# Performance work log

Hardware: AMD Instinct MI355X
Metric: run time of the kernel (lower is better)

The kernel has to match this reference:

```python
import jax, jax.numpy as jnp
import numpy as np
import math

N_HEAD = 4
NORM_GROUPS = 16
EPS = 1e-5


def setup_inputs() -> dict:
    key = jax.random.key(0)
    ks = jax.random.split(key, 4)
    B, C, H, W = 2, 256, 64, 64
    return {
        "input": jax.random.normal(ks[0], (B, C, H, W), dtype=jnp.float32),
        "gn_weight": jnp.ones((C,), dtype=jnp.float32),
        "gn_bias": jnp.zeros((C,), dtype=jnp.float32),
        # 1x1 convs are plain channel matmuls: weight [out_ch, in_ch]
        "qkv_weight": jax.random.normal(ks[1], (3 * C, C), dtype=jnp.float32) / math.sqrt(C),
        "out_weight": jax.random.normal(ks[2], (C, C), dtype=jnp.float32) / math.sqrt(C),
        "out_bias": jnp.zeros((C,), dtype=jnp.float32),
    }


def _group_norm(x, weight, bias):
    B, C, H, W = x.shape
    g = x.reshape(B, NORM_GROUPS, C // NORM_GROUPS, H, W)
    mu = g.mean(axis=(2, 3, 4), keepdims=True)
    var = g.var(axis=(2, 3, 4), keepdims=True)
    g = (g - mu) * jax.lax.rsqrt(var + EPS)
    return g.reshape(B, C, H, W) * weight[:, None, None] + bias[:, None, None]


def reference(input, gn_weight, gn_bias, qkv_weight, out_weight, out_bias):
    B, C, H, W = input.shape
    head_dim = C // N_HEAD
    x = _group_norm(input, gn_weight, gn_bias)
    # 1x1 conv (no bias) -> [B, 3C, H, W] -> [B, n_head, 3*head_dim, H, W]
    qkv = jnp.einsum('bchw,oc->bohw', x, qkv_weight)
    qkv = qkv.reshape(B, N_HEAD, 3 * head_dim, H, W)
    q, k, v = jnp.split(qkv, 3, axis=2)
    # full spatial attention; note: scale is sqrt(channel), as in the source
    attn = jnp.einsum('bnchw,bncyx->bnhwyx', q, k) / math.sqrt(C)
    attn = jax.nn.softmax(attn.reshape(B, N_HEAD, H, W, H * W), axis=-1)
    attn = attn.reshape(B, N_HEAD, H, W, H, W)
    out = jnp.einsum('bnhwyx,bncyx->bnchw', attn, v).reshape(B, C, H, W)
    out = jnp.einsum('bchw,oc->bohw', out, out_weight) + out_bias[:, None, None]
    return out + input
```

## Files before the change

### kernel.cpp

```cpp
#include <hip/hip_runtime.h>

typedef __bf16        bf16x8 __attribute__((ext_vector_type(8)));
typedef float         f32x4  __attribute__((ext_vector_type(4)));
typedef unsigned short u16x4 __attribute__((ext_vector_type(4)));
typedef unsigned short u16x8 __attribute__((ext_vector_type(8)));
typedef unsigned int  u32x4  __attribute__((ext_vector_type(4)));

#define MFMA16(a,b,c) __builtin_amdgcn_mfma_f32_16x16x32_bf16((a),(b),(c),0,0,0)

static __device__ __forceinline__ unsigned short f2bf(float f) {
  unsigned int u = __builtin_bit_cast(unsigned int, f);
  u += 0x7fffu + ((u >> 16) & 1u);
  return (unsigned short)(u >> 16);
}
static __device__ __forceinline__ unsigned int pk2(float a, float b) {
  unsigned int ua = __builtin_bit_cast(unsigned int, a) + 0x8000u;
  unsigned int ub = __builtin_bit_cast(unsigned int, b) + 0x8000u;
  return __builtin_amdgcn_perm(ub, ua, 0x07060302u);
}
static __device__ __forceinline__ unsigned int pk2rne(float a, float b) {
  return (unsigned int)f2bf(a) | ((unsigned int)f2bf(b) << 16);
}
static __device__ __forceinline__ bf16x8 as_bf(u32x4 v) {
  return __builtin_bit_cast(bf16x8, v);
}
static __device__ __forceinline__ float bf2f(unsigned short u) {
  return __builtin_bit_cast(float, ((unsigned int)u) << 16);
}
static __device__ __forceinline__ void dma16(const unsigned short* g, unsigned short* l) {
  __builtin_amdgcn_global_load_lds((const __attribute__((address_space(1))) unsigned int*)g,
                                   (__attribute__((address_space(3))) unsigned int*)l, 16, 0, 0);
}

#define SDIM 4096
#define CDIM 256
#define NHEAD 4
#define HDIM 64
#define NBATCH 2
#define KSPLIT 4

__global__ __launch_bounds__(256) void k_prep(const float* __restrict__ x,
                                              const float* __restrict__ wq,
                                              const float* __restrict__ wo,
                                              unsigned short* __restrict__ wqb,
                                              unsigned short* __restrict__ wob,
                                              float2* __restrict__ Sp) {
  int j = blockIdx.x, i = threadIdx.x;
  if (j < 256) {
    const float* p = x + (size_t)(j >> 3) * 65536 + (size_t)(j & 7) * 8192;
    float s = 0.f, sq = 0.f;
#pragma unroll
    for (int r = 0; r < 8; ++r) {
      float4 v = *(const float4*)(p + (r * 256 + i) * 4);
      s  += v.x + v.y + v.z + v.w;
      sq += v.x * v.x + v.y * v.y + v.z * v.z + v.w * v.w;
    }
    __shared__ float rs[256], rq[256];
    rs[i] = s; rq[i] = sq;
    __syncthreads();
    for (int off = 128; off > 0; off >>= 1) {
      if (i < off) { rs[i] += rs[i + off]; rq[i] += rq[i + off]; }
      __syncthreads();
    }
    if (i == 0) Sp[j] = make_float2(rs[0], rq[0]);
  } else {
    int t = (j - 256) * 256 + i;
    int e = t * 16;
#pragma unroll
    for (int c = 0; c < 4; ++c) {
      int idx = e + c * 4;
      const float* src = (idx < 768 * 256) ? (wq + idx) : (wo + idx - 768 * 256);
      unsigned short* dst = (idx < 768 * 256) ? (wqb + idx) : (wob + idx - 768 * 256);
      float4 v = *(const float4*)src;
      u16x4 r; r[0] = f2bf(v.x); r[1] = f2bf(v.y); r[2] = f2bf(v.z); r[3] = f2bf(v.w);
      *(u16x4*)dst = r;
    }
  }
}

__global__ __launch_bounds__(256) void k_gn_apply(const float* __restrict__ x,
                                                  const float2* __restrict__ Sp,
                                                  const float* __restrict__ gnw,
                                                  const float* __restrict__ gnb,
                                                  unsigned short* __restrict__ xn) {
  __shared__ __attribute__((aligned(16))) unsigned short sT[64 * 268];
  __shared__ float2 sStat[16];
  int b = blockIdx.y, s0 = blockIdx.x * 64;
  int i = threadIdx.x, lane = i & 63, w = i >> 6;
  if (i < 16) {
    float s = 0.f, sq = 0.f;
#pragma unroll
    for (int u = 0; u < 8; ++u) {
      float2 v = Sp[(b * 16 + i) * 8 + u];
      s += v.x; sq += v.y;
    }
    float mean = s * (1.f / 65536.f);
    float var  = sq * (1.f / 65536.f) - mean * mean;
    sStat[i] = make_float2(mean, rsqrtf(var + 1e-5f));
  }
  __syncthreads();
#pragma unroll 4
  for (int r = 0; r < 64; ++r) {
    int c = r * 4 + w;
    float v = x[((size_t)(b * CDIM + c)) * SDIM + s0 + lane];
    float2 st = sStat[c >> 4];
    float nv = (v - st.x) * st.y * gnw[c] + gnb[c];
    sT[lane * 268 + c] = f2bf(nv);
  }
  __syncthreads();
#pragma unroll
  for (int r = 0; r < 16; ++r) {
    int sl = r * 4 + w;
    u16x4 v = *(const u16x4*)&sT[sl * 268 + lane * 4];
    *(u16x4*)&xn[((size_t)(b * SDIM + s0 + sl)) * CDIM + lane * 4] = v;
  }
}

template <int M, int MODE>
__global__ __launch_bounds__(256) void k_gemm(const unsigned short* __restrict__ W,
                                              const unsigned short* __restrict__ X,
                                              unsigned short* __restrict__ Qf,
                                              unsigned short* __restrict__ Kf,
                                              unsigned short* __restrict__ Vf,
                                              float* __restrict__ outf,
                                              const float* __restrict__ bias,
                                              const float* __restrict__ resid) {
  __shared__ __attribute__((aligned(16))) unsigned short sX[64 * 40];
  __shared__ __attribute__((aligned(16))) unsigned short sB[64 * 68];
  int b = blockIdx.z, s0 = blockIdx.y * 64, o0 = blockIdx.x * 64;
  int i = threadIdx.x, lane = i & 63, w = i >> 6;
  int quad = lane >> 4, m = lane & 15;
  const unsigned short* Xb = X + ((size_t)b * SDIM + s0) * CDIM;
  int ss = i >> 2, cq = i & 3;

  f32x4 acc[4] = {};
#pragma unroll
  for (int k0 = 0; k0 < 256; k0 += 32) {
    u32x4 xv = *(const u32x4*)(Xb + ss * CDIM + k0 + cq * 8);
    *(u32x4*)&sX[ss * 40 + cq * 8] = xv;
    __syncthreads();
    bf16x8 a = as_bf(*(const u32x4*)(W + (o0 + w * 16 + m) * 256 + k0 + quad * 8));
#pragma unroll
    for (int st = 0; st < 4; ++st) {
      bf16x8 bx = as_bf(*(const u32x4*)&sX[(st * 16 + m) * 40 + quad * 8]);
      acc[st] = MFMA16(a, bx, acc[st]);
    }
    __syncthreads();
  }
  if (MODE == 1) {
#pragma unroll
    for (int st = 0; st < 4; ++st)
#pragma unroll
      for (int r = 0; r < 4; ++r) {
        int o = o0 + w * 16 + quad * 4 + r;
        int s = s0 + st * 16 + m;
        size_t idx = ((size_t)b * M + o) * SDIM + s;
        outf[idx] = acc[st][r] + bias[o] + resid[idx];
      }
  } else {
    int sec = (o0 >> 6) % 3;
    int h   = o0 / 192;
    int bh  = b * NHEAD + h;
    float qs = (sec == 0) ? 0.09016844f : 1.0f;
#pragma unroll
    for (int st = 0; st < 4; ++st) {
      uint2 pk = make_uint2(pk2rne(acc[st][0] * qs, acc[st][1] * qs),
                            pk2rne(acc[st][2] * qs, acc[st][3] * qs));
      *(uint2*)&sB[(st * 16 + m) * 68 + w * 16 + quad * 4] = pk;
    }
    __syncthreads();
    int lp = i & 63, qp = lp >> 4, mp = lp & 15, t = i >> 6;
    if (sec < 2) {
      unsigned short* base = (sec == 0) ? Qf : Kf;
#pragma unroll
      for (int ks = 0; ks < 2; ++ks) {
        const unsigned short* src = &sB[(t * 16 + mp) * 68 + ks * 32 + qp * 8];
        u16x4 lo = *(const u16x4*)src;
        u16x4 hi = *(const u16x4*)(src + 4);
        unsigned short* dst = base + ((((size_t)bh * 256 + (s0 >> 4) + t) * 2 + ks) * 64 + lp) * 8;
        *(u16x4*)dst = lo;
        *(u16x4*)(dst + 4) = hi;
      }
    } else {
      int kt32l = t >> 1, dts = (t & 1) * 2;
#pragma unroll
      for (int dd = 0; dd < 2; ++dd) {
        int dt = dts + dd;
        u16x8 v;
#pragma unroll
        for (int jj = 0; jj < 8; ++jj)
          v[jj] = sB[(kt32l * 32 + qp * 8 + jj) * 68 + dt * 16 + mp];
        unsigned short* dst = Vf + ((((size_t)bh * 128 + (s0 >> 5) + kt32l) * 4 + dt) * 64 + lp) * 8;
        *(u16x8*)dst = v;
      }
    }
  }
}

__global__ __launch_bounds__(256, 4) void k_attn(const unsigned short* __restrict__ Qf,
                                                 const unsigned short* __restrict__ Kf,
                                                 const unsigned short* __restrict__ Vf,
                                                 unsigned short* __restrict__ Opb,
                                                 float* __restrict__ Lp) {
  __shared__ __attribute__((aligned(16))) unsigned short sK[2][2048];
  __shared__ __attribute__((aligned(16))) unsigned short sV[2][2048];
  __shared__ __attribute__((aligned(16))) unsigned short sP[4][32 * 40];
  int bh = blockIdx.y, kk = blockIdx.z;
  int i = threadIdx.x, lane = i & 63, w = i >> 6;
  int quad = lane >> 4, m = lane & 15;
  constexpr int ITERS = SDIM / KSPLIT / 32;

  bf16x8 bq[2][2];
#pragma unroll
  for (int qt = 0; qt < 2; ++qt)
#pragma unroll
    for (int ks = 0; ks < 2; ++ks)
      bq[qt][ks] = as_bf(*(const u32x4*)(Qf +
        ((((size_t)bh * 256 + (blockIdx.x * 8 + w * 2 + qt)) * 2 + ks) * 64 + lane) * 8));

  f32x4 oacc[2][4] = {};
  float li[2] = {0.f, 0.f};

  auto dma = [&](int it, int buf) {
    int kb16 = kk * (ITERS * 2) + it * 2 + (w >> 1);
    dma16(Kf + ((((size_t)bh * 256 + kb16) * 2 + (w & 1)) * 64 + lane) * 8,
          &sK[buf][w * 512]);
    int kb32 = kk * ITERS + it;
    dma16(Vf + ((((size_t)bh * 128 + kb32) * 4 + w) * 64 + lane) * 8,
          &sV[buf][w * 512]);
  };
  dma(0, 0);

  for (int it = 0; it < ITERS; ++it) {
    int buf = it & 1;
    __syncthreads();
    if (it < ITERS - 1) dma(it + 1, buf ^ 1);

    {
      bf16x8 ak[2][2];
#pragma unroll
      for (int ky = 0; ky < 2; ++ky)
#pragma unroll
        for (int ks = 0; ks < 2; ++ks)
          ak[ky][ks] = *(const bf16x8*)&sK[buf][((ky * 2 + ks) * 64 + lane) * 8];
#pragma unroll
      for (int qt = 0; qt < 2; ++qt) {
        f32x4 sc0 = {-18.f, -18.f, -18.f, -18.f};
        f32x4 sc1 = sc0;
        sc0 = MFMA16(ak[0][0], bq[qt][0], sc0);
        sc0 = MFMA16(ak[0][1], bq[qt][1], sc0);
        sc1 = MFMA16(ak[1][0], bq[qt][0], sc1);
        sc1 = MFMA16(ak[1][1], bq[qt][1], sc1);
        float p[8];
#pragma unroll
        for (int r = 0; r < 4; ++r) {
          p[r]     = __builtin_amdgcn_exp2f(sc0[r]);
          p[4 + r] = __builtin_amdgcn_exp2f(sc1[r]);
        }
        li[qt] += ((p[0] + p[1]) + (p[2] + p[3])) + ((p[4] + p[5]) + (p[6] + p[7]));
        int row = (qt * 16 + m) * 40;
        *(uint2*)&sP[w][row + quad * 4]      = make_uint2(pk2(p[0], p[1]), pk2(p[2], p[3]));
        *(uint2*)&sP[w][row + 16 + quad * 4] = make_uint2(pk2(p[4], p[5]), pk2(p[6], p[7]));
      }
    }
    {
      bf16x8 av[4];
#pragma unroll
      for (int dt = 0; dt < 4; ++dt)
        av[dt] = *(const bf16x8*)&sV[buf][(dt * 64 + lane) * 8];
#pragma unroll
      for (int qt = 0; qt < 2; ++qt) {
        bf16x8 bp = *(const bf16x8*)&sP[w][(qt * 16 + m) * 40 + quad * 8];
#pragma unroll
        for (int dt = 0; dt < 4; ++dt)
          oacc[qt][dt] = MFMA16(av[dt], bp, oacc[qt][dt]);
      }
    }
  }

  size_t qg = (size_t)(kk * 8 + bh) * SDIM + blockIdx.x * 128 + w * 32;
#pragma unroll
  for (int qt = 0; qt < 2; ++qt) {
    li[qt] += __shfl_xor(li[qt], 16);
    li[qt] += __shfl_xor(li[qt], 32);
  }
  if (quad == 0) {
#pragma unroll
    for (int qt = 0; qt < 2; ++qt) Lp[qg + qt * 16 + m] = li[qt];
  }
#pragma unroll
  for (int qt = 0; qt < 2; ++qt)
#pragma unroll
    for (int dt = 0; dt < 4; ++dt) {
      uint2 pk = make_uint2(pk2rne(oacc[qt][dt][0], oacc[qt][dt][1]),
                            pk2rne(oacc[qt][dt][2], oacc[qt][dt][3]));
      *(uint2*)&Opb[(qg + qt * 16 + m) * 64 + dt * 16 + quad * 4] = pk;
    }
}

__global__ __launch_bounds__(256) void k_combine(const unsigned short* __restrict__ Opb,
                                                 const float* __restrict__ Lp,
                                                 unsigned short* __restrict__ ao) {
  int gid = blockIdx.x * 256 + threadIdx.x;
  int bh = gid >> 14, rem = gid & 16383, q = rem >> 2, dq = rem & 3;
  float li = 0.f, o[16];
#pragma unroll
  for (int e = 0; e < 16; ++e) o[e] = 0.f;
#pragma unroll
  for (int ks = 0; ks < KSPLIT; ++ks) {
    size_t base = (size_t)(ks * 8 + bh) * SDIM + q;
    li += Lp[base];
    const unsigned short* p = Opb + base * 64 + dq * 16;
    u16x8 a = *(const u16x8*)p, b2 = *(const u16x8*)(p + 8);
#pragma unroll
    for (int e = 0; e < 8; ++e) { o[e] += bf2f(a[e]); o[8 + e] += bf2f(b2[e]); }
  }
  float inv = 1.f / li;
  unsigned int dw[8];
#pragma unroll
  for (int e = 0; e < 8; ++e) dw[e] = pk2rne(o[2 * e] * inv, o[2 * e + 1] * inv);
  unsigned short* dst = ao + ((size_t)((bh >> 2) * SDIM + q)) * CDIM + (bh & 3) * HDIM + dq * 16;
  *(u32x4*)dst       = u32x4{dw[0], dw[1], dw[2], dw[3]};
  *(u32x4*)(dst + 8) = u32x4{dw[4], dw[5], dw[6], dw[7]};
}

extern "C" void kernel_launch(void* const* d_in, const int* in_sizes, int n_in,
                              void* d_out, int out_size, void* d_ws, size_t ws_size,
                              hipStream_t stream) {
  const float* input = (const float*)d_in[0];
  const float* gnw   = (const float*)d_in[1];
  const float* gnb   = (const float*)d_in[2];
  const float* wq    = (const float*)d_in[3];
  const float* wo    = (const float*)d_in[4];
  const float* ob    = (const float*)d_in[5];
  float* out = (float*)d_out;

  char* ws = (char*)d_ws;
  unsigned short* xn  = (unsigned short*)(ws);
  unsigned short* Qf  = (unsigned short*)(ws + (4ull  << 20));
  unsigned short* Kf  = (unsigned short*)(ws + (8ull  << 20));
  unsigned short* Vf  = (unsigned short*)(ws + (12ull << 20));
  unsigned short* ao  = (unsigned short*)(ws + (16ull << 20));
  unsigned short* wqb = (unsigned short*)(ws + (20ull << 20));
  unsigned short* wob = (unsigned short*)(ws + (20ull << 20) + (1u << 19));
  float2* Sp          = (float2*)(ws + (20ull << 20) + (3u << 18));
  float* Lp           = (float*)(ws + (21ull << 20));
  unsigned short* Opb = (unsigned short*)(ws + (22ull << 20));

  k_prep<<<320, 256, 0, stream>>>(input, wq, wo, wqb, wob, Sp);
  k_gn_apply<<<dim3(64, NBATCH), 256, 0, stream>>>(input, Sp, gnw, gnb, xn);
  k_gemm<768, 0><<<dim3(12, 64, NBATCH), 256, 0, stream>>>(wqb, xn, Qf, Kf, Vf, nullptr, nullptr, nullptr);
  k_attn<<<dim3(32, NHEAD * NBATCH, KSPLIT), 256, 0, stream>>>(Qf, Kf, Vf, Opb, Lp);
  k_combine<<<512, 256, 0, stream>>>(Opb, Lp, ao);
  k_gemm<256, 1><<<dim3(4, 64, NBATCH), 256, 0, stream>>>(wob, ao, nullptr, nullptr, nullptr, out, ob, input);
}
```

Baseline: 147.0 us.

## Pre-swizzle operands into MFMA fragment layout and drop LDS staging

Weights, normalized activations and attention output are now written in a per-lane MFMA fragment layout, so the GEMMs load operands straight from global memory with no LDS staging or barriers. The attention kernel drops its double-buffered global-to-LDS K/V prefetch in favour of direct fragment loads. It computes the softmax row sum with an extra MFMA against a ones vector, which removes the exp-sum adds and cross-lane shuffles. It also uses the hardware packed bf16 conversion when available. In exchange, K/V global loads are no longer overlapped with compute, and the row sum is now taken from bf16-rounded probabilities.

```diff
diff --git a/kernel.cpp b/kernel.cpp
--- a/kernel.cpp
+++ b/kernel.cpp
@@ -13,23 +13,22 @@
   u += 0x7fffu + ((u >> 16) & 1u);
   return (unsigned short)(u >> 16);
 }
-static __device__ __forceinline__ unsigned int pk2(float a, float b) {
-  unsigned int ua = __builtin_bit_cast(unsigned int, a) + 0x8000u;
-  unsigned int ub = __builtin_bit_cast(unsigned int, b) + 0x8000u;
-  return __builtin_amdgcn_perm(ub, ua, 0x07060302u);
-}
 static __device__ __forceinline__ unsigned int pk2rne(float a, float b) {
   return (unsigned int)f2bf(a) | ((unsigned int)f2bf(b) << 16);
 }
+static __device__ __forceinline__ unsigned int pkrn(float a, float b) {
+#if __has_builtin(__builtin_amdgcn_cvt_pk_bf16_f32)
+  auto r = __builtin_amdgcn_cvt_pk_bf16_f32(a, b);
+  return __builtin_bit_cast(unsigned int, r);
+#else
+  return pk2rne(a, b);
+#endif
+}
 static __device__ __forceinline__ bf16x8 as_bf(u32x4 v) {
   return __builtin_bit_cast(bf16x8, v);
 }
 static __device__ __forceinline__ float bf2f(unsigned short u) {
   return __builtin_bit_cast(float, ((unsigned int)u) << 16);
-}
-static __device__ __forceinline__ void dma16(const unsigned short* g, unsigned short* l) {
-  __builtin_amdgcn_global_load_lds((const __attribute__((address_space(1))) unsigned int*)g,
-                                   (__attribute__((address_space(3))) unsigned int*)l, 16, 0, 0);
 }
 
 #define SDIM 4096
@@ -42,8 +41,8 @@
 __global__ __launch_bounds__(256) void k_prep(const float* __restrict__ x,
                                               const float* __restrict__ wq,
                                               const float* __restrict__ wo,
-                                              unsigned short* __restrict__ wqb,
-                                              unsigned short* __restrict__ wob,
+                                              unsigned short* __restrict__ wqf,
+                                              unsigned short* __restrict__ wof,
                                               float2* __restrict__ Sp) {
   int j = blockIdx.x, i = threadIdx.x;
   if (j < 256) {
@@ -65,15 +64,24 @@
     if (i == 0) Sp[j] = make_float2(rs[0], rq[0]);
   } else {
     int t = (j - 256) * 256 + i;
-    int e = t * 16;
-#pragma unroll
-    for (int c = 0; c < 4; ++c) {
-      int idx = e + c * 4;
-      const float* src = (idx < 768 * 256) ? (wq + idx) : (wo + idx - 768 * 256);
-      unsigned short* dst = (idx < 768 * 256) ? (wqb + idx) : (wob + idx - 768 * 256);
-      float4 v = *(const float4*)src;
-      u16x4 r; r[0] = f2bf(v.x); r[1] = f2bf(v.y); r[2] = f2bf(v.z); r[3] = f2bf(v.w);
-      *(u16x4*)dst = r;
+#pragma unroll
+    for (int u = 0; u < 2; ++u) {
+      int G = t * 2 + u;
+      const float* src; unsigned short* dst;
+      if (G < 24576) {
+        int tile = G >> 6, l = G & 63;
+        src = wq + (size_t)((tile >> 3) * 16 + (l & 15)) * 256 + (tile & 7) * 32 + (l >> 4) * 8;
+        dst = wqf + (size_t)G * 8;
+      } else {
+        int G2 = G - 24576, tile = G2 >> 6, l = G2 & 63;
+        src = wo + (size_t)((tile >> 3) * 16 + (l & 15)) * 256 + (tile & 7) * 32 + (l >> 4) * 8;
+        dst = wof + (size_t)G2 * 8;
+      }
+      float4 v0 = *(const float4*)src, v1 = *(const float4*)(src + 4);
+      u16x8 r;
+      r[0] = f2bf(v0.x); r[1] = f2bf(v0.y); r[2] = f2bf(v0.z); r[3] = f2bf(v0.w);
+      r[4] = f2bf(v1.x); r[5] = f2bf(v1.y); r[6] = f2bf(v1.z); r[7] = f2bf(v1.w);
+      *(u16x8*)dst = r;
     }
   }
 }
@@ -82,7 +90,7 @@
                                                   const float2* __restrict__ Sp,
                                                   const float* __restrict__ gnw,
                                                   const float* __restrict__ gnb,
-                                                  unsigned short* __restrict__ xn) {
+                                                  unsigned short* __restrict__ Xf) {
   __shared__ __attribute__((aligned(16))) unsigned short sT[64 * 268];
   __shared__ float2 sStat[16];
   int b = blockIdx.y, s0 = blockIdx.x * 64;
@@ -108,45 +116,45 @@
     sT[lane * 268 + c] = f2bf(nv);
   }
   __syncthreads();
-#pragma unroll
-  for (int r = 0; r < 16; ++r) {
-    int sl = r * 4 + w;
-    u16x4 v = *(const u16x4*)&sT[sl * 268 + lane * 4];
-    *(u16x4*)&xn[((size_t)(b * SDIM + s0 + sl)) * CDIM + lane * 4] = v;
+  int l = i & 63, fr = i >> 6;
+#pragma unroll
+  for (int g = 0; g < 8; ++g) {
+    int tile = fr * 8 + g, st = tile >> 3, kc = tile & 7;
+    const unsigned short* src = &sT[(st * 16 + (l & 15)) * 268 + kc * 32 + (l >> 4) * 8];
+    u16x4 lo = *(const u16x4*)src, hi = *(const u16x4*)(src + 4);
+    unsigned short* dst = Xf + (((size_t)(b * 256 + (s0 >> 4) + st) * 8 + kc) * 64 + l) * 8;
+    *(u16x4*)dst = lo;
+    *(u16x4*)(dst + 4) = hi;
   }
 }
 
 template <int M, int MODE>
-__global__ __launch_bounds__(256) void k_gemm(const unsigned short* __restrict__ W,
-                                              const unsigned short* __restrict__ X,
+__global__ __launch_bounds__(256) void k_gemm(const unsigned short* __restrict__ Wf,
+                                              const unsigned short* __restrict__ Xf,
                                               unsigned short* __restrict__ Qf,
                                               unsigned short* __restrict__ Kf,
                                               unsigned short* __restrict__ Vf,
                                               float* __restrict__ outf,
                                               const float* __restrict__ bias,
                                               const float* __restrict__ resid) {
-  __shared__ __attribute__((aligned(16))) unsigned short sX[64 * 40];
   __shared__ __attribute__((aligned(16))) unsigned short sB[64 * 68];
   int b = blockIdx.z, s0 = blockIdx.y * 64, o0 = blockIdx.x * 64;
   int i = threadIdx.x, lane = i & 63, w = i >> 6;
   int quad = lane >> 4, m = lane & 15;
-  const unsigned short* Xb = X + ((size_t)b * SDIM + s0) * CDIM;
-  int ss = i >> 2, cq = i & 3;
+  int ot = blockIdx.x * 4 + w;
+  int stg = s0 >> 4;
 
   f32x4 acc[4] = {};
 #pragma unroll
-  for (int k0 = 0; k0 < 256; k0 += 32) {
-    u32x4 xv = *(const u32x4*)(Xb + ss * CDIM + k0 + cq * 8);
-    *(u32x4*)&sX[ss * 40 + cq * 8] = xv;
-    __syncthreads();
-    bf16x8 a = as_bf(*(const u32x4*)(W + (o0 + w * 16 + m) * 256 + k0 + quad * 8));
+  for (int kc = 0; kc < 8; ++kc) {
+    bf16x8 aW = as_bf(*(const u32x4*)(Wf + (((size_t)ot * 8 + kc) * 64 + lane) * 8));
 #pragma unroll
     for (int st = 0; st < 4; ++st) {
-      bf16x8 bx = as_bf(*(const u32x4*)&sX[(st * 16 + m) * 40 + quad * 8]);
-      acc[st] = MFMA16(a, bx, acc[st]);
-    }
-    __syncthreads();
-  }
+      bf16x8 bX = as_bf(*(const u32x4*)(Xf + ((((size_t)b * 256 + stg + st) * 8 + kc) * 64 + lane) * 8));
+      acc[st] = MFMA16(aW, bX, acc[st]);
+    }
+  }
+
   if (MODE == 1) {
 #pragma unroll
     for (int st = 0; st < 4; ++st)
@@ -202,8 +210,6 @@
                                                  const unsigned short* __restrict__ Vf,
                                                  unsigned short* __restrict__ Opb,
                                                  float* __restrict__ Lp) {
-  __shared__ __attribute__((aligned(16))) unsigned short sK[2][2048];
-  __shared__ __attribute__((aligned(16))) unsigned short sV[2][2048];
   __shared__ __attribute__((aligned(16))) unsigned short sP[4][32 * 40];
   int bh = blockIdx.y, kk = blockIdx.z;
   int i = threadIdx.x, lane = i & 63, w = i >> 6;
@@ -218,75 +224,64 @@
       bq[qt][ks] = as_bf(*(const u32x4*)(Qf +
         ((((size_t)bh * 256 + (blockIdx.x * 8 + w * 2 + qt)) * 2 + ks) * 64 + lane) * 8));
 
+  bf16x8 aone;
+  {
+    u16x8 t;
+#pragma unroll
+    for (int jj = 0; jj < 8; ++jj) t[jj] = 0x3F80;
+    aone = __builtin_bit_cast(bf16x8, t);
+  }
+
   f32x4 oacc[2][4] = {};
-  float li[2] = {0.f, 0.f};
-
-  auto dma = [&](int it, int buf) {
-    int kb16 = kk * (ITERS * 2) + it * 2 + (w >> 1);
-    dma16(Kf + ((((size_t)bh * 256 + kb16) * 2 + (w & 1)) * 64 + lane) * 8,
-          &sK[buf][w * 512]);
+  f32x4 liacc[2] = {};
+
+  for (int it = 0; it < ITERS; ++it) {
+    bf16x8 ak[2][2], av[4];
+    int kb16 = kk * (ITERS * 2) + it * 2;
+#pragma unroll
+    for (int ky = 0; ky < 2; ++ky)
+#pragma unroll
+      for (int ks = 0; ks < 2; ++ks)
+        ak[ky][ks] = as_bf(*(const u32x4*)(Kf +
+          ((((size_t)bh * 256 + kb16 + ky) * 2 + ks) * 64 + lane) * 8));
     int kb32 = kk * ITERS + it;
-    dma16(Vf + ((((size_t)bh * 128 + kb32) * 4 + w) * 64 + lane) * 8,
-          &sV[buf][w * 512]);
-  };
-  dma(0, 0);
-
-  for (int it = 0; it < ITERS; ++it) {
-    int buf = it & 1;
-    __syncthreads();
-    if (it < ITERS - 1) dma(it + 1, buf ^ 1);
-
-    {
-      bf16x8 ak[2][2];
-#pragma unroll
-      for (int ky = 0; ky < 2; ++ky)
-#pragma unroll
-        for (int ks = 0; ks < 2; ++ks)
-          ak[ky][ks] = *(const bf16x8*)&sK[buf][((ky * 2 + ks) * 64 + lane) * 8];
-#pragma unroll
-      for (int qt = 0; qt < 2; ++qt) {
-        f32x4 sc0 = {-18.f, -18.f, -18.f, -18.f};
-        f32x4 sc1 = sc0;
-        sc0 = MFMA16(ak[0][0], bq[qt][0], sc0);
-        sc0 = MFMA16(ak[0][1], bq[qt][1], sc0);
-        sc1 = MFMA16(ak[1][0], bq[qt][0], sc1);
-        sc1 = MFMA16(ak[1][1], bq[qt][1], sc1);
-        float p[8];
-#pragma unroll
-        for (int r = 0; r < 4; ++r) {
-          p[r]     = __builtin_amdgcn_exp2f(sc0[r]);
-          p[4 + r] = __builtin_amdgcn_exp2f(sc1[r]);
-        }
-        li[qt] += ((p[0] + p[1]) + (p[2] + p[3])) + ((p[4] + p[5]) + (p[6] + p[7]));
-        int row = (qt * 16 + m) * 40;
-        *(uint2*)&sP[w][row + quad * 4]      = make_uint2(pk2(p[0], p[1]), pk2(p[2], p[3]));
-        *(uint2*)&sP[w][row + 16 + quad * 4] = make_uint2(pk2(p[4], p[5]), pk2(p[6], p[7]));
-      }
-    }
-    {
-      bf16x8 av[4];
+#pragma unroll
+    for (int dt = 0; dt < 4; ++dt)
+      av[dt] = as_bf(*(const u32x4*)(Vf +
+        ((((size_t)bh * 128 + kb32) * 4 + dt) * 64 + lane) * 8));
+
+#pragma unroll
+    for (int qt = 0; qt < 2; ++qt) {
+      f32x4 sc0 = {-18.f, -18.f, -18.f, -18.f};
+      f32x4 sc1 = sc0;
+      sc0 = MFMA16(ak[0][0], bq[qt][0], sc0);
+      sc0 = MFMA16(ak[0][1], bq[qt][1], sc0);
+      sc1 = MFMA16(ak[1][0], bq[qt][0], sc1);
+      sc1 = MFMA16(ak[1][1], bq[qt][1], sc1);
+      float p[8];
+#pragma unroll
+      for (int r = 0; r < 4; ++r) {
+        p[r]     = __builtin_amdgcn_exp2f(sc0[r]);
+        p[4 + r] = __builtin_amdgcn_exp2f(sc1[r]);
+      }
+      int row = (qt * 16 + m) * 40;
+      *(uint2*)&sP[w][row + quad * 4]      = make_uint2(pkrn(p[0], p[1]), pkrn(p[2], p[3]));
+      *(uint2*)&sP[w][row + 16 + quad * 4] = make_uint2(pkrn(p[4], p[5]), pkrn(p[6], p[7]));
+    }
+#pragma unroll
+    for (int qt = 0; qt < 2; ++qt) {
+      bf16x8 bp = *(const bf16x8*)&sP[w][(qt * 16 + m) * 40 + quad * 8];
 #pragma unroll
       for (int dt = 0; dt < 4; ++dt)
-        av[dt] = *(const bf16x8*)&sV[buf][(dt * 64 + lane) * 8];
-#pragma unroll
-      for (int qt = 0; qt < 2; ++qt) {
-        bf16x8 bp = *(const bf16x8*)&sP[w][(qt * 16 + m) * 40 + quad * 8];
-#pragma unroll
-        for (int dt = 0; dt < 4; ++dt)
-          oacc[qt][dt] = MFMA16(av[dt], bp, oacc[qt][dt]);
-      }
+        oacc[qt][dt] = MFMA16(av[dt], bp, oacc[qt][dt]);
+      liacc[qt] = MFMA16(aone, bp, liacc[qt]);
     }
   }
 
   size_t qg = (size_t)(kk * 8 + bh) * SDIM + blockIdx.x * 128 + w * 32;
-#pragma unroll
-  for (int qt = 0; qt < 2; ++qt) {
-    li[qt] += __shfl_xor(li[qt], 16);
-    li[qt] += __shfl_xor(li[qt], 32);
-  }
   if (quad == 0) {
 #pragma unroll
-    for (int qt = 0; qt < 2; ++qt) Lp[qg + qt * 16 + m] = li[qt];
+    for (int qt = 0; qt < 2; ++qt) Lp[qg + qt * 16 + m] = liacc[qt][0];
   }
 #pragma unroll
   for (int qt = 0; qt < 2; ++qt)
@@ -300,7 +295,7 @@
 
 __global__ __launch_bounds__(256) void k_combine(const unsigned short* __restrict__ Opb,
                                                  const float* __restrict__ Lp,
-                                                 unsigned short* __restrict__ ao) {
+                                                 unsigned short* __restrict__ aof) {
   int gid = blockIdx.x * 256 + threadIdx.x;
   int bh = gid >> 14, rem = gid & 16383, q = rem >> 2, dq = rem & 3;
   float li = 0.f, o[16];
@@ -319,9 +314,11 @@
   unsigned int dw[8];
 #pragma unroll
   for (int e = 0; e < 8; ++e) dw[e] = pk2rne(o[2 * e] * inv, o[2 * e + 1] * inv);
-  unsigned short* dst = ao + ((size_t)((bh >> 2) * SDIM + q)) * CDIM + (bh & 3) * HDIM + dq * 16;
-  *(u32x4*)dst       = u32x4{dw[0], dw[1], dw[2], dw[3]};
-  *(u32x4*)(dst + 8) = u32x4{dw[4], dw[5], dw[6], dw[7]};
+  int b = bh >> 2, c0 = (bh & 3) * 64 + dq * 16;
+  int st = q >> 4, mm = q & 15, kc = c0 >> 5, qd = (c0 >> 3) & 3;
+  unsigned short* base = aof + (((size_t)(b * 256 + st) * 8 + kc) * 64) * 8;
+  *(u32x4*)(base + (qd * 16 + mm) * 8)       = u32x4{dw[0], dw[1], dw[2], dw[3]};
+  *(u32x4*)(base + ((qd + 1) * 16 + mm) * 8) = u32x4{dw[4], dw[5], dw[6], dw[7]};
 }
 
 extern "C" void kernel_launch(void* const* d_in, const int* in_sizes, int n_in,
@@ -336,21 +333,21 @@
   float* out = (float*)d_out;
 
   char* ws = (char*)d_ws;
-  unsigned short* xn  = (unsigned short*)(ws);
+  unsigned short* Xf  = (unsigned short*)(ws);
   unsigned short* Qf  = (unsigned short*)(ws + (4ull  << 20));
   unsigned short* Kf  = (unsigned short*)(ws + (8ull  << 20));
   unsigned short* Vf  = (unsigned short*)(ws + (12ull << 20));
-  unsigned short* ao  = (unsigned short*)(ws + (16ull << 20));
-  unsigned short* wqb = (unsigned short*)(ws + (20ull << 20));
-  unsigned short* wob = (unsigned short*)(ws + (20ull << 20) + (1u << 19));
+  unsigned short* aof = (unsigned short*)(ws + (16ull << 20));
+  unsigned short* wqf = (unsigned short*)(ws + (20ull << 20));
+  unsigned short* wof = (unsigned short*)(ws + (20ull << 20) + (1u << 19));
   float2* Sp          = (float2*)(ws + (20ull << 20) + (3u << 18));
   float* Lp           = (float*)(ws + (21ull << 20));
   unsigned short* Opb = (unsigned short*)(ws + (22ull << 20));
 
-  k_prep<<<320, 256, 0, stream>>>(input, wq, wo, wqb, wob, Sp);
-  k_gn_apply<<<dim3(64, NBATCH), 256, 0, stream>>>(input, Sp, gnw, gnb, xn);
-  k_gemm<768, 0><<<dim3(12, 64, NBATCH), 256, 0, stream>>>(wqb, xn, Qf, Kf, Vf, nullptr, nullptr, nullptr);
+  k_prep<<<320, 256, 0, stream>>>(input, wq, wo, wqf, wof, Sp);
+  k_gn_apply<<<dim3(64, NBATCH), 256, 0, stream>>>(input, Sp, gnw, gnb, Xf);
+  k_gemm<768, 0><<<dim3(12, 64, NBATCH), 256, 0, stream>>>(wqf, Xf, Qf, Kf, Vf, nullptr, nullptr, nullptr);
   k_attn<<<dim3(32, NHEAD * NBATCH, KSPLIT), 256, 0, stream>>>(Qf, Kf, Vf, Opb, Lp);
-  k_combine<<<512, 256, 0, stream>>>(Opb, Lp, ao);
-  k_gemm<256, 1><<<dim3(4, 64, NBATCH), 256, 0, stream>>>(wob, ao, nullptr, nullptr, nullptr, out, ob, input);
-}
+  k_combine<<<512, 256, 0, stream>>>(Opb, Lp, aof);
+  k_gemm<256, 1><<<dim3(4, 64, NBATCH), 256, 0, stream>>>(wof, aof, nullptr, nullptr, nullptr, out, ob, input);
+}
```

Result: no change. 148.5 us (+1.0%).
